# Kernel tuning notes

Measured on AMD Instinct MI355X. Metric: run time of the kernel, lower is better.

## Reference

```python
import jax, jax.numpy as jnp
import numpy as np

TOTAL_BITS = 16
FRAC_BITS = 8
SCALE = float(2 ** FRAC_BITS)
MINV = -(2.0 ** (TOTAL_BITS - 1)) / SCALE          # -128.0
MAXV = (2.0 ** (TOTAL_BITS - 1) - 1.0) / SCALE     # 127.99609375
BN_EPS = 1e-5


def fp_quantize(x):
    """Fixed-point fake-quant: clamp to representable range, round to nearest
    multiple of 2^-frac_bits. Rounding uses straight-through estimator (matches
    the repo's RoundToFixedPoint autograd)."""
    x = jnp.clip(x, MINV, MAXV)
    r = jnp.round(x * SCALE) / SCALE
    return x + jax.lax.stop_gradient(r - x)


def setup_inputs() -> dict:
    key = jax.random.key(0)
    k1, k2, k3 = jax.random.split(key, 3)
    B, IN, OUT = 8192, 2048, 2048
    x = jax.random.normal(k1, (B, IN), dtype=jnp.float32)
    # realistic init scale so fixed-point range is exercised but not saturated
    weight = jax.random.normal(k2, (OUT, IN), dtype=jnp.float32) * 0.02
    bias = jax.random.normal(k3, (OUT,), dtype=jnp.float32) * 0.02
    gamma = jnp.ones((OUT,), dtype=jnp.float32)
    beta = jnp.zeros((OUT,), dtype=jnp.float32)
    return {"x": x, "weight": weight, "bias": bias, "gamma": gamma, "beta": beta}


def reference(x, weight, bias, gamma, beta):
    # fixed-point Linear: quantize params, quantized matmul, quantized add
    qw = fp_quantize(weight)            # [OUT, IN]
    qb = fp_quantize(bias)              # [OUT]
    y = fp_quantize(x @ qw.T)           # [B, OUT], arithmetics.matmul
    y = fp_quantize(y + qb)             # arithmetics.add
    # BatchNorm1d, training mode: biased batch statistics over the batch dim
    mean = jnp.mean(y, axis=0)
    var = jnp.mean((y - mean) ** 2, axis=0)
    y = (y - mean) * jax.lax.rsqrt(var + BN_EPS)
    y = gamma * y + beta
    # final quantize of BN output
    return fp_quantize(y)
```

## Files before the change

kernel.cpp:

```cpp
#include <hip/hip_runtime.h>
#include <hip/hip_bf16.h>

#define Mdim 8192
#define Ndim 2048
#define Kdim 2048
#define NT   32

constexpr float kMin = -128.0f;
constexpr float kMax = 127.99609375f;
constexpr float kScale = 256.0f;
constexpr float kInvScale = 1.0f / 256.0f;
constexpr float kEps = 1e-5f;

typedef __attribute__((ext_vector_type(8))) short short8;
typedef __attribute__((ext_vector_type(4))) float f32x4;

__device__ __forceinline__ float fpq(float x) {
    x = fminf(fmaxf(x, kMin), kMax);
    return rintf(x * kScale) * kInvScale;
}

__device__ __forceinline__ unsigned short f2bf(float f) {
    union { __hip_bfloat16 h; unsigned short u; } cv;
    cv.h = __float2bfloat16(f);
    return cv.u;
}

__device__ __forceinline__ void gload_lds16(const void* g, void* l) {
    __builtin_amdgcn_global_load_lds(
        (const __attribute__((address_space(1))) unsigned int*)g,
        (__attribute__((address_space(3))) unsigned int*)l,
        16, 0, 0);
}

__device__ __forceinline__ void phase_barrier() {
    __builtin_amdgcn_sched_barrier(0);
    __builtin_amdgcn_s_barrier();
    __builtin_amdgcn_sched_barrier(0);
    asm volatile("" ::: "memory");
}

__device__ __forceinline__ void wait_vmcnt4() {
    __builtin_amdgcn_sched_barrier(0);
    asm volatile("s_waitcnt vmcnt(4)" ::: "memory");
    __builtin_amdgcn_sched_barrier(0);
}

__global__ void fpbn_prep(const float* __restrict__ w,
                          unsigned short* __restrict__ wb,
                          const float* __restrict__ x,
                          unsigned short* __restrict__ xb,
                          float* __restrict__ stats) {
    const int b = blockIdx.x;
    if (b == 0) {
        float4 z = {0.f, 0.f, 0.f, 0.f};
        for (int i = threadIdx.x; i < 1024; i += 256)
            ((float4*)stats)[i] = z;
    }
    if (b < 1024) {
        const int n4 = Ndim * Kdim / 4;
        for (int i = b * 256 + threadIdx.x; i < n4; i += 1024 * 256) {
            float4 v = ((const float4*)w)[i];
            ushort4 o;
            o.x = f2bf(fpq(v.x));
            o.y = f2bf(fpq(v.y));
            o.z = f2bf(fpq(v.z));
            o.w = f2bf(fpq(v.w));
            ((ushort4*)wb)[i] = o;
        }
    } else {
        const int n8 = Mdim * Kdim / 8;
        for (int i = (b - 1024) * 256 + threadIdx.x; i < n8; i += 2048 * 256) {
            float4 p = ((const float4*)x)[2 * i];
            float4 q = ((const float4*)x)[2 * i + 1];
            uint4 o;
            o.x = (unsigned)f2bf(p.x) | ((unsigned)f2bf(p.y) << 16);
            o.y = (unsigned)f2bf(p.z) | ((unsigned)f2bf(p.w) << 16);
            o.z = (unsigned)f2bf(q.x) | ((unsigned)f2bf(q.y) << 16);
            o.w = (unsigned)f2bf(q.z) | ((unsigned)f2bf(q.w) << 16);
            ((uint4*)xb)[i] = o;
        }
    }
}

template <bool OUT16>
__global__ __launch_bounds__(512, 2) void fpbn_gemm8(
    const unsigned short* __restrict__ xb, const unsigned short* __restrict__ wb,
    const float* __restrict__ bias, short* __restrict__ y16,
    float* __restrict__ yf, float* __restrict__ colsum,
    float* __restrict__ colsumsq) {

    __shared__ unsigned short lds[65536];

    const int t    = threadIdx.x;
    const int lane = t & 63;
    const int w    = t >> 6;
    const int wm   = w >> 2;
    const int wn   = w & 3;

    const int blk  = blockIdx.x;
    const int bm   = (blk & 7) * 4 + (blk >> 6);
    const int bn   = (blk >> 3) & 7;
    const int row0 = bm * 256;
    const int col0 = bn * 256;

    const int roff = t >> 3;
    const int colE = ((t & 7) ^ (roff & 7)) * 8;
    const unsigned short* srcA[2] = {
        xb + (size_t)(row0 +   0 + roff) * Kdim + colE,
        xb + (size_t)(row0 + 128 + roff) * Kdim + colE };
    const unsigned short* srcB[2] = {
        wb + (size_t)(col0 +   0 + roff) * Kdim + colE,
        wb + (size_t)(col0 + 128 + roff) * Kdim + colE };
    const int t8 = t * 8;

    const int x3    = lane & 7;
    const int xk    = x3 >> 2;
    const int xh    = x3 & 3;
    const int hi    = lane >> 4;
    const int rb2   = (lane & 15) * 64 + ((hi ^ xh) * 8);
    const int k0off = xk * 32;
    const int k1off = 32 - k0off;
    const int bnoff = (wn & 1) * 4096;

#define STAGE(BUF_, S_, OP_, HALF_) do {                                      \
        int ss_ = (S_) < NT ? (S_) : (S_) - 2;  \
        const unsigned short* sp_ = (OP_ ? srcB : srcA)[HALF_] + ss_ * 64;    \
        unsigned short* dp_ =                                                 \
            &lds[(((BUF_) * 4 + (OP_) * 2 + (HALF_)) << 13) + t8];            \
        gload_lds16(sp_, dp_);                                                \
        gload_lds16(sp_ + (size_t)64 * Kdim, dp_ + 4096);                     \
    } while (0)

#define READA(BUF_, M_, KOFF_) \
    (*(const short8*)&lds[(((BUF_) * 4 + wm) << 13) + rb2 + (M_) * 1024 + (KOFF_)])
#define READB(BUF_, N_, KOFF_) \
    (*(const short8*)&lds[(((BUF_) * 4 + 2 + (wn >> 1)) << 13) + bnoff + rb2 + (N_) * 1024 + (KOFF_)])
#define MFMA_(A_, B_, C_) \
    C_ = __builtin_amdgcn_mfma_f32_16x16x32_bf16(A_, B_, C_, 0, 0, 0)

    f32x4 acc[8][4] = {};

    STAGE(0, 0, 0, 0); STAGE(0, 0, 0, 1); STAGE(0, 0, 1, 0); STAGE(0, 0, 1, 1);
    STAGE(1, 1, 0, 0); STAGE(1, 1, 0, 1);
    __builtin_amdgcn_sched_barrier(0);
    asm volatile("s_waitcnt vmcnt(0)" ::: "memory");
    __builtin_amdgcn_sched_barrier(0);
    phase_barrier();

#define KTILE(BUF_, ST1_, ST2_, ST3_, ST4_) do {                              \
                                                        \
        _Pragma("unroll") for (int n = 0; n < 2; ++n) {                       \
            Bf0[n][0] = READB(BUF_, n, k0off);                                \
            Bf0[n][1] = READB(BUF_, n, k1off); }                              \
        _Pragma("unroll") for (int m = 0; m < 4; ++m) {                       \
            Af[m][0] = READA(BUF_, m, k0off);                                 \
            Af[m][1] = READA(BUF_, m, k1off); }                               \
        ST1_;                                                                 \
        __builtin_amdgcn_s_setprio(1);                                        \
        _Pragma("unroll") for (int m = 0; m < 4; ++m)                         \
        _Pragma("unroll") for (int n = 0; n < 2; ++n) {                       \
            MFMA_(Af[m][0], Bf0[n][0], acc[m][n]);                            \
            MFMA_(Af[m][1], Bf0[n][1], acc[m][n]); }                          \
        __builtin_amdgcn_s_setprio(0);                                        \
        phase_barrier();                                                      \
                \
        _Pragma("unroll") for (int n = 0; n < 2; ++n) {                       \
            Bf1[n][0] = READB(BUF_, n + 2, k0off);                            \
            Bf1[n][1] = READB(BUF_, n + 2, k1off); }                          \
        _Pragma("unroll") for (int m = 0; m < 4; ++m) {                       \
            Af2[m][0] = READA(BUF_, m + 4, k0off);                            \
            Af2[m][1] = READA(BUF_, m + 4, k1off); }                          \
        ST2_;                                                                 \
        __builtin_amdgcn_s_setprio(1);                                        \
        _Pragma("unroll") for (int m = 0; m < 4; ++m)                         \
        _Pragma("unroll") for (int n = 0; n < 2; ++n) {                       \
            MFMA_(Af[m][0], Bf1[n][0], acc[m][n + 2]);                        \
            MFMA_(Af[m][1], Bf1[n][1], acc[m][n + 2]); }                      \
        __builtin_amdgcn_s_setprio(0);                                        \
        phase_barrier();                                                      \
                                                                      \
        ST3_;                                                                 \
        __builtin_amdgcn_s_setprio(1);                                        \
        _Pragma("unroll") for (int m = 0; m < 4; ++m)                         \
        _Pragma("unroll") for (int n = 0; n < 2; ++n) {                       \
            MFMA_(Af2[m][0], Bf1[n][0], acc[m + 4][n + 2]);                   \
            MFMA_(Af2[m][1], Bf1[n][1], acc[m + 4][n + 2]); }                 \
        __builtin_amdgcn_s_setprio(0);                                        \
        phase_barrier();                                                      \
                                         \
        ST4_;                                                                 \
        wait_vmcnt4();                                                        \
        phase_barrier();                                                      \
        __builtin_amdgcn_s_setprio(1);                                        \
        _Pragma("unroll") for (int m = 0; m < 4; ++m)                         \
        _Pragma("unroll") for (int n = 0; n < 2; ++n) {                       \
            MFMA_(Af2[m][0], Bf0[n][0], acc[m + 4][n]);                       \
            MFMA_(Af2[m][1], Bf0[n][1], acc[m + 4][n]); }                     \
        __builtin_amdgcn_s_setprio(0);                                        \
    } while (0)

#pragma unroll 1
    for (int it = 0; it < NT / 2; ++it) {
        const int s0 = 2 * it;
        short8 Af[4][2], Af2[4][2], Bf0[2][2], Bf1[2][2];
        KTILE(0, STAGE(1, s0 + 1, 1, 0), STAGE(1, s0 + 1, 1, 1),
                 STAGE(0, s0 + 2, 0, 0), STAGE(0, s0 + 2, 0, 1));
        KTILE(1, STAGE(0, s0 + 2, 1, 0), STAGE(0, s0 + 2, 1, 1),
                 STAGE(1, s0 + 3, 0, 0), STAGE(1, s0 + 3, 0, 1));
    }

#pragma unroll
    for (int n = 0; n < 4; ++n) {
        const int col = col0 + wn * 64 + n * 16 + (lane & 15);
        const float qb = fpq(bias[col]);
        float s = 0.0f, s2 = 0.0f;
#pragma unroll
        for (int m = 0; m < 8; ++m) {
            const int rowb = row0 + wm * 128 + m * 16 + ((lane >> 4) * 4);
#pragma unroll
            for (int j = 0; j < 4; ++j) {
                float v = fpq(acc[m][n][j]);
                v = fpq(v + qb);
                if constexpr (OUT16) {
                    size_t idx = ((((size_t)blk * 8 + w) * 4 + n) * 32
                                  + m * 4 + j) * 64 + lane;
                    y16[idx] = (short)(v * 256.0f);
                } else {
                    yf[(size_t)(rowb + j) * Ndim + col] = v;
                }
                s += v;
                s2 += v * v;
            }
        }
        s  += __shfl_xor(s, 16, 64);  s  += __shfl_xor(s, 32, 64);
        s2 += __shfl_xor(s2, 16, 64); s2 += __shfl_xor(s2, 32, 64);
        if (lane < 16) {
            atomicAdd(&colsum[col], s);
            atomicAdd(&colsumsq[col], s2);
        }
    }
#undef STAGE
#undef READA
#undef READB
#undef MFMA_
#undef KTILE
}

__global__ void fpbn_finalize(const float* __restrict__ colsum,
                              const float* __restrict__ colsumsq,
                              const float* __restrict__ gamma,
                              const float* __restrict__ beta,
                              float* __restrict__ a, float* __restrict__ b) {
    int i = blockIdx.x * blockDim.x + threadIdx.x;
    if (i < Ndim) {
        float mean = colsum[i] * (1.0f / Mdim);
        float var  = colsumsq[i] * (1.0f / Mdim) - mean * mean;
        float inv  = 1.0f / sqrtf(var + kEps);
        float ai   = gamma[i] * inv;
        a[i] = ai;
        b[i] = beta[i] - mean * ai;
    }
}

__global__ void fpbn_apply16(const short* __restrict__ y16,
                             float* __restrict__ out,
                             const float* __restrict__ a,
                             const float* __restrict__ b, int ngroups) {
    int tid = blockIdx.x * blockDim.x + threadIdx.x;
    int stride = gridDim.x * blockDim.x;
    for (int g = tid; g < ngroups; g += stride) {
        const int r  = g >> 8;
        const int c  = (g & 255) * 8;
        const int bm = r >> 8, wm = (r >> 7) & 1, m = (r >> 4) & 7,
                  hi = (r >> 2) & 3, j = r & 3;
        const int bn = c >> 8, wn = (c >> 6) & 3, n = (c >> 4) & 3,
                  lane = hi * 16 + (c & 15);
        const int blk = (bm >> 2) | (bn << 3) | ((bm & 3) << 6);
        const int w   = wm * 4 + wn;
        const size_t idx = ((((size_t)blk * 8 + w) * 4 + n) * 32
                            + m * 4 + j) * 64 + lane;
        int4 raw = *(const int4*)(y16 + idx);
        const short* sp = (const short*)&raw;
        float4 a0 = *(const float4*)&a[c], a1 = *(const float4*)&a[c + 4];
        float4 b0 = *(const float4*)&b[c], b1 = *(const float4*)&b[c + 4];
        float4 o0, o1;
        o0.x = fpq(fmaf(a0.x, (float)sp[0] * kInvScale, b0.x));
        o0.y = fpq(fmaf(a0.y, (float)sp[1] * kInvScale, b0.y));
        o0.z = fpq(fmaf(a0.z, (float)sp[2] * kInvScale, b0.z));
        o0.w = fpq(fmaf(a0.w, (float)sp[3] * kInvScale, b0.w));
        o1.x = fpq(fmaf(a1.x, (float)sp[4] * kInvScale, b1.x));
        o1.y = fpq(fmaf(a1.y, (float)sp[5] * kInvScale, b1.y));
        o1.z = fpq(fmaf(a1.z, (float)sp[6] * kInvScale, b1.z));
        o1.w = fpq(fmaf(a1.w, (float)sp[7] * kInvScale, b1.w));
        float* op = out + (size_t)r * Ndim + c;
        ((float4*)op)[0] = o0;
        ((float4*)op)[1] = o1;
    }
}

__global__ void fpbn_apply(float* __restrict__ y,
                           const float* __restrict__ a,
                           const float* __restrict__ b, int n4) {
    int i = blockIdx.x * blockDim.x + threadIdx.x;
    int stride = gridDim.x * blockDim.x;
    for (; i < n4; i += stride) {
        float4 v = ((float4*)y)[i];
        int cb = (i * 4) & (Ndim - 1);
        float4 av = *(const float4*)&a[cb];
        float4 bv = *(const float4*)&b[cb];
        v.x = fpq(fmaf(av.x, v.x, bv.x));
        v.y = fpq(fmaf(av.y, v.y, bv.y));
        v.z = fpq(fmaf(av.z, v.z, bv.z));
        v.w = fpq(fmaf(av.w, v.w, bv.w));
        ((float4*)y)[i] = v;
    }
}

extern "C" void kernel_launch(void* const* d_in, const int* in_sizes, int n_in,
                              void* d_out, int out_size, void* d_ws, size_t ws_size,
                              hipStream_t stream) {
    const float* x      = (const float*)d_in[0];
    const float* weight = (const float*)d_in[1];
    const float* bias   = (const float*)d_in[2];
    const float* gamma  = (const float*)d_in[3];
    const float* beta   = (const float*)d_in[4];
    float* out = (float*)d_out;

    char* ws = (char*)d_ws;
    unsigned short* wb = (unsigned short*)ws;
    const size_t wbBytes = (size_t)Ndim * Kdim * 2;
    float* colsum   = (float*)(ws + wbBytes);
    float* colsumsq = colsum + Ndim;
    float* aArr     = colsum + 2 * Ndim;
    float* bArr     = colsum + 3 * Ndim;
    const size_t xbOff = wbBytes + 65536;
    unsigned short* xb = (unsigned short*)(ws + xbOff);
    const size_t xbBytes  = (size_t)Mdim * Kdim * 2;
    const size_t y16Off   = xbOff + xbBytes;
    short* y16 = (short*)(ws + y16Off);
    const size_t need16 = y16Off + (size_t)Mdim * Ndim * 2;

    fpbn_prep<<<3072, 256, 0, stream>>>(weight, wb, x, xb, colsum);

    if (ws_size >= need16) {
        fpbn_gemm8<true><<<(Mdim / 256) * (Ndim / 256), 512, 0, stream>>>(
            xb, wb, bias, y16, nullptr, colsum, colsumsq);
        fpbn_finalize<<<(Ndim + 255) / 256, 256, 0, stream>>>(
            colsum, colsumsq, gamma, beta, aArr, bArr);
        fpbn_apply16<<<2048, 256, 0, stream>>>(y16, out, aArr, bArr,
                                               Mdim * Ndim / 8);
    } else {
        fpbn_gemm8<false><<<(Mdim / 256) * (Ndim / 256), 512, 0, stream>>>(
            xb, wb, bias, nullptr, out, colsum, colsumsq);
        fpbn_finalize<<<(Ndim + 255) / 256, 256, 0, stream>>>(
            colsum, colsumsq, gamma, beta, aArr, bArr);
        fpbn_apply<<<2048, 256, 0, stream>>>(out, aArr, bArr, Mdim * Ndim / 4);
    }
}
```

Baseline: 230.1 us.

## Restructure GEMM K-loop into finer barrier phases with deeper prefetch gating

Reorganizes the bf16 MFMA main loop so each K-tile runs four phases, each opened by a barrier plus lgkmcnt wait and closed by a barrier. The global-to-LDS stage order is reshuffled so B tiles are prefetched further ahead and the prologue issues seven stages gated by vmcnt(6) rather than a full vmcnt(0) drain. The aim is to keep more loads in flight and interleave LDS reads with MFMA work, cutting stalls on memory. This adds more barriers per tile and relies on subtle buffer-reuse ordering that could introduce races or extra synchronization cost.

```diff
diff --git a/kernel.cpp b/kernel.cpp
--- a/kernel.cpp
+++ b/kernel.cpp
@@ -31,19 +31,6 @@
         (const __attribute__((address_space(1))) unsigned int*)g,
         (__attribute__((address_space(3))) unsigned int*)l,
         16, 0, 0);
-}
-
-__device__ __forceinline__ void phase_barrier() {
-    __builtin_amdgcn_sched_barrier(0);
-    __builtin_amdgcn_s_barrier();
-    __builtin_amdgcn_sched_barrier(0);
-    asm volatile("" ::: "memory");
-}
-
-__device__ __forceinline__ void wait_vmcnt4() {
-    __builtin_amdgcn_sched_barrier(0);
-    asm volatile("s_waitcnt vmcnt(4)" ::: "memory");
-    __builtin_amdgcn_sched_barrier(0);
 }
 
 __global__ void fpbn_prep(const float* __restrict__ w,
@@ -139,76 +126,85 @@
 #define MFMA_(A_, B_, C_) \
     C_ = __builtin_amdgcn_mfma_f32_16x16x32_bf16(A_, B_, C_, 0, 0, 0)
 
+#define PH_OPEN                                                    \
+    __builtin_amdgcn_s_barrier();                                  \
+    asm volatile("s_waitcnt lgkmcnt(0)" ::: "memory");             \
+    __builtin_amdgcn_sched_barrier(0);                             \
+    __builtin_amdgcn_s_setprio(1);
+
+#define PH_CLOSE                                                   \
+    __builtin_amdgcn_s_setprio(0);                                 \
+    __builtin_amdgcn_s_barrier();
+
+#define GATE_VM6 asm volatile("s_waitcnt vmcnt(6)" ::: "memory")
+
     f32x4 acc[8][4] = {};
 
-    STAGE(0, 0, 0, 0); STAGE(0, 0, 0, 1); STAGE(0, 0, 1, 0); STAGE(0, 0, 1, 1);
-    STAGE(1, 1, 0, 0); STAGE(1, 1, 0, 1);
-    __builtin_amdgcn_sched_barrier(0);
-    asm volatile("s_waitcnt vmcnt(0)" ::: "memory");
-    __builtin_amdgcn_sched_barrier(0);
-    phase_barrier();
-
-#define KTILE(BUF_, ST1_, ST2_, ST3_, ST4_) do {                              \
-                                                        \
+    STAGE(0, 0, 1, 0); STAGE(0, 0, 1, 1); STAGE(0, 0, 0, 0); STAGE(0, 0, 0, 1);
+    STAGE(1, 1, 1, 0); STAGE(1, 1, 1, 1); STAGE(1, 1, 0, 0);
+    GATE_VM6;
+    __builtin_amdgcn_s_barrier();
+
+#define KTILE(BUF_, SA1_, SB0_, SB1_, SA0_) do {                              \
+                                     \
         _Pragma("unroll") for (int n = 0; n < 2; ++n) {                       \
             Bf0[n][0] = READB(BUF_, n, k0off);                                \
             Bf0[n][1] = READB(BUF_, n, k1off); }                              \
         _Pragma("unroll") for (int m = 0; m < 4; ++m) {                       \
             Af[m][0] = READA(BUF_, m, k0off);                                 \
             Af[m][1] = READA(BUF_, m, k1off); }                               \
-        ST1_;                                                                 \
-        __builtin_amdgcn_s_setprio(1);                                        \
+        SA1_;                                                                 \
+        PH_OPEN                                                               \
         _Pragma("unroll") for (int m = 0; m < 4; ++m)                         \
         _Pragma("unroll") for (int n = 0; n < 2; ++n) {                       \
             MFMA_(Af[m][0], Bf0[n][0], acc[m][n]);                            \
             MFMA_(Af[m][1], Bf0[n][1], acc[m][n]); }                          \
-        __builtin_amdgcn_s_setprio(0);                                        \
-        phase_barrier();                                                      \
-                \
+        PH_CLOSE                                                              \
+                                              \
         _Pragma("unroll") for (int n = 0; n < 2; ++n) {                       \
             Bf1[n][0] = READB(BUF_, n + 2, k0off);                            \
             Bf1[n][1] = READB(BUF_, n + 2, k1off); }                          \
+        PH_OPEN                                                               \
+        _Pragma("unroll") for (int m = 0; m < 4; ++m)                         \
+        _Pragma("unroll") for (int n = 0; n < 2; ++n) {                       \
+            MFMA_(Af[m][0], Bf1[n][0], acc[m][n + 2]);                        \
+            MFMA_(Af[m][1], Bf1[n][1], acc[m][n + 2]); }                      \
+        PH_CLOSE                                                              \
+              \
         _Pragma("unroll") for (int m = 0; m < 4; ++m) {                       \
             Af2[m][0] = READA(BUF_, m + 4, k0off);                            \
             Af2[m][1] = READA(BUF_, m + 4, k1off); }                          \
-        ST2_;                                                                 \
-        __builtin_amdgcn_s_setprio(1);                                        \
-        _Pragma("unroll") for (int m = 0; m < 4; ++m)                         \
-        _Pragma("unroll") for (int n = 0; n < 2; ++n) {                       \
-            MFMA_(Af[m][0], Bf1[n][0], acc[m][n + 2]);                        \
-            MFMA_(Af[m][1], Bf1[n][1], acc[m][n + 2]); }                      \
-        __builtin_amdgcn_s_setprio(0);                                        \
-        phase_barrier();                                                      \
-                                                                      \
-        ST3_;                                                                 \
-        __builtin_amdgcn_s_setprio(1);                                        \
+        SB0_;                                                                 \
+        SB1_;                                                                 \
+        PH_OPEN                                                               \
         _Pragma("unroll") for (int m = 0; m < 4; ++m)                         \
         _Pragma("unroll") for (int n = 0; n < 2; ++n) {                       \
             MFMA_(Af2[m][0], Bf1[n][0], acc[m + 4][n + 2]);                   \
             MFMA_(Af2[m][1], Bf1[n][1], acc[m + 4][n + 2]); }                 \
-        __builtin_amdgcn_s_setprio(0);                                        \
-        phase_barrier();                                                      \
-                                         \
-        ST4_;                                                                 \
-        wait_vmcnt4();                                                        \
-        phase_barrier();                                                      \
-        __builtin_amdgcn_s_setprio(1);                                        \
+        PH_CLOSE                                                              \
+            \
+        SA0_;                                                                 \
+        GATE_VM6;                                                             \
+        PH_OPEN                                                               \
         _Pragma("unroll") for (int m = 0; m < 4; ++m)                         \
         _Pragma("unroll") for (int n = 0; n < 2; ++n) {                       \
             MFMA_(Af2[m][0], Bf0[n][0], acc[m + 4][n]);                       \
             MFMA_(Af2[m][1], Bf0[n][1], acc[m + 4][n]); }                     \
-        __builtin_amdgcn_s_setprio(0);                                        \
+        PH_CLOSE                                                              \
     } while (0)
 
 #pragma unroll 1
     for (int it = 0; it < NT / 2; ++it) {
         const int s0 = 2 * it;
         short8 Af[4][2], Af2[4][2], Bf0[2][2], Bf1[2][2];
-        KTILE(0, STAGE(1, s0 + 1, 1, 0), STAGE(1, s0 + 1, 1, 1),
-                 STAGE(0, s0 + 2, 0, 0), STAGE(0, s0 + 2, 0, 1));
-        KTILE(1, STAGE(0, s0 + 2, 1, 0), STAGE(0, s0 + 2, 1, 1),
-                 STAGE(1, s0 + 3, 0, 0), STAGE(1, s0 + 3, 0, 1));
-    }
+        KTILE(0, STAGE(1, s0 + 1, 0, 1),
+                 STAGE(0, s0 + 2, 1, 0), STAGE(0, s0 + 2, 1, 1),
+                 STAGE(0, s0 + 2, 0, 0));
+        KTILE(1, STAGE(0, s0 + 2, 0, 1),
+                 STAGE(1, s0 + 3, 1, 0), STAGE(1, s0 + 3, 1, 1),
+                 STAGE(1, s0 + 3, 0, 0));
+    }
+    asm volatile("s_waitcnt vmcnt(0)" ::: "memory");
 
 #pragma unroll
     for (int n = 0; n < 4; ++n) {
@@ -245,6 +241,9 @@
 #undef READB
 #undef MFMA_
 #undef KTILE
+#undef PH_OPEN
+#undef PH_CLOSE
+#undef GATE_VM6
 }
 
 __global__ void fpbn_finalize(const float* __restrict__ colsum,
```

Result: faster. 215.5 us (-6.3%).
